# Kernel tuning notes

Measured on AMD Instinct MI355X. Metric: run time of the kernel, lower is better.

Reference implementation:

```python
import jax, jax.numpy as jnp
import numpy as np

# ---- module constants (from init_kwargs) ----
EMBED_DIM = 384
NUM_HYPEREDGES = 128
TOPK = 64
SPATIAL_SHAPE = (16, 32, 32)  # D, H, W -> N = 16384
SPACING = (2.0, 1.0, 1.0)
SPATIAL_WEIGHT = 0.1
B, N, C = 4, 16 * 32 * 32, EMBED_DIM


def _l2norm(x, axis=-1, eps=1e-12):
    n = jnp.linalg.norm(x, axis=axis, keepdims=True)
    return x / jnp.maximum(n, eps)


def _get_3d_coords():
    D, H, W = SPATIAL_SHAPE
    z = jnp.arange(D, dtype=jnp.float32) * SPACING[0]
    y = jnp.arange(H, dtype=jnp.float32) * SPACING[1]
    x = jnp.arange(W, dtype=jnp.float32) * SPACING[2]
    zz, yy, xx = jnp.meshgrid(z, y, x, indexing='ij')
    return jnp.stack([zz, yy, xx], axis=-1).reshape(-1, 3)  # (N, 3)


def setup_inputs() -> dict:
    key = jax.random.key(0)
    k1, k2 = jax.random.split(key)
    node_features = jax.random.normal(k1, (B, N, C), dtype=jnp.float32)
    class_token = jax.random.normal(k2, (1, 1, C), dtype=jnp.float32)
    temperature = jnp.ones((1,), dtype=jnp.float32) * 0.07
    return {"node_features": node_features, "class_token": class_token, "temperature": temperature}


def reference(node_features, class_token, temperature):
    Ne = NUM_HYPEREDGES
    w = SPATIAL_WEIGHT
    temp = temperature[0]

    nodes_n = _l2norm(node_features)                      # (B, N, C)

    # Step 1: center sampling by semantic similarity to class token
    ct_n = _l2norm(jnp.broadcast_to(class_token, (B, 1, C)))
    scores = jnp.einsum('boc,bnc->bn', ct_n, nodes_n) / temp  # (B, N)
    _, center_idx = jax.lax.top_k(scores, Ne)             # (B, Ne)

    # Gather centers and compute cosine sim of every center vs all nodes
    centers = jnp.take_along_axis(node_features, center_idx[:, :, None], axis=1)  # (B, Ne, C)
    centers_n = _l2norm(centers)
    sem_sim = jnp.einsum('bec,bnc->ben', centers_n, nodes_n) / temp  # (B, Ne, N)

    # Spatial bias (normalized distance from each center voxel)
    coords = _get_3d_coords()                             # (N, 3)
    center_coords = coords[center_idx]                    # (B, Ne, 3)
    diff = coords[None, None, :, :] - center_coords[:, :, None, :]  # (B, Ne, N, 3)
    dist = jnp.linalg.norm(diff, axis=-1)                 # (B, Ne, N)
    dist = dist / (jnp.max(dist, axis=-1, keepdims=True) + 1e-8)
    combined = (1.0 - w) * sem_sim + w * (1.0 - dist)     # (B, Ne, N)

    # Per-hyperedge top-K neighbors -> incidence matrix H (B, N, Ne)
    _, nbr_idx = jax.lax.top_k(combined, TOPK)            # (B, Ne, K)
    b_ix = jnp.arange(B)[:, None, None]
    e_ix = jnp.arange(Ne)[None, :, None]
    Hmat = jnp.zeros((B, N, Ne), dtype=node_features.dtype)
    Hmat = Hmat.at[b_ix, nbr_idx, e_ix].set(1.0)
    return Hmat
```

## Files before the change

kernel.cpp:

```cpp
#include <hip/hip_runtime.h>
#include <math.h>

#define BB 4
#define NN 16384
#define CC 384
#define NE 128
#define KK 64
#define CAP 1024

typedef unsigned short ushort_t;
typedef __attribute__((ext_vector_type(8))) short bf16x8;
typedef __attribute__((ext_vector_type(4))) float f32x4;
#define MFMA(a, b, c) __builtin_amdgcn_mfma_f32_16x16x32_bf16(a, b, c, 0, 0, 0)

__device__ inline unsigned fkey(float f) {
    unsigned b = __float_as_uint(f);
    return (b & 0x80000000u) ? ~b : (b | 0x80000000u);
}
__device__ inline ushort_t bf16rne(float f) {
    unsigned u = __float_as_uint(f);
    unsigned r = u + 0x7FFFu + ((u >> 16) & 1u);
    return (ushort_t)(r >> 16);
}
__device__ inline float bf16tof(ushort_t h) {
    return __uint_as_float(((unsigned)h) << 16);
}
__device__ inline void cvt2(float fa, float fb, unsigned& hp, unsigned& lp) {
    unsigned ua = __float_as_uint(fa), ub = __float_as_uint(fb);
    unsigned ra = ua + 0x8000u, rb = ub + 0x8000u;
    hp = (ra >> 16) | (rb & 0xFFFF0000u);
    float ha = __uint_as_float(ra & 0xFFFF0000u);
    float hb = __uint_as_float(rb & 0xFFFF0000u);
    float la = fa - ha, lb = fb - hb;
    unsigned lra = __float_as_uint(la) + 0x8000u;
    unsigned lrb = __float_as_uint(lb) + 0x8000u;
    lp = (lra >> 16) | (lrb & 0xFFFF0000u);
}

__device__ inline void load_lds16(const ushort_t* g, ushort_t* l) {
    __builtin_amdgcn_global_load_lds(
        (const __attribute__((address_space(1))) unsigned int*)(const void*)g,
        (__attribute__((address_space(3))) unsigned int*)(void*)l, 16, 0, 0);
}

__device__ inline void bin_select4k(const unsigned* hist, int t, int* wsum,
                                    int* sh_bin, int* sh_r, int r) {
    int base = t * 4;
    int c0 = hist[base], c1 = hist[base + 1], c2 = hist[base + 2], c3 = hist[base + 3];
    int csum = c0 + c1 + c2 + c3;
    int lane = t & 63, wid = t >> 6;
    int x = csum;
#pragma unroll
    for (int off = 1; off < 64; off <<= 1) {
        int v = __shfl_down(x, off, 64);
        if (lane + off < 64) x += v;
    }
    if (lane == 0) wsum[wid] = x;
    __syncthreads();
    int after = 0;
    for (int w2 = wid + 1; w2 < 16; ++w2) after += wsum[w2];
    int S = x - csum + after;
    if (S < r && S + c3 >= r) { *sh_bin = base + 3; *sh_r = r - S; }
    S += c3;
    if (S < r && S + c2 >= r) { *sh_bin = base + 2; *sh_r = r - S; }
    S += c2;
    if (S < r && S + c1 >= r) { *sh_bin = base + 1; *sh_r = r - S; }
    S += c1;
    if (S < r && S + c0 >= r) { *sh_bin = base + 0; *sh_r = r - S; }
    __syncthreads();
}

__global__ __launch_bounds__(256) void k_scores(const float* __restrict__ nf,
                                                const float* __restrict__ ct,
                                                unsigned* __restrict__ keys,
                                                float* __restrict__ invn) {
    int wave = threadIdx.x >> 6;
    int lane = threadIdx.x & 63;
    int row  = blockIdx.x * 4 + wave;
    const float* x = nf + (size_t)row * CC;
    float4 a  = ((const float4*)x)[lane];
    float2 c2 = ((const float2*)(x + 256))[lane];
    float4 ta = ((const float4*)ct)[lane];
    float2 tc = ((const float2*)(ct + 256))[lane];
    float ss = a.x*a.x + a.y*a.y + a.z*a.z + a.w*a.w + c2.x*c2.x + c2.y*c2.y;
    float dt = ta.x*a.x + ta.y*a.y + ta.z*a.z + ta.w*a.w + tc.x*c2.x + tc.y*c2.y;
#pragma unroll
    for (int off = 32; off; off >>= 1) {
        ss += __shfl_xor(ss, off, 64);
        dt += __shfl_xor(dt, off, 64);
    }
    if (lane == 0) {
        float inv = 1.0f / fmaxf(sqrtf(ss), 1e-12f);
        invn[row] = inv;
        keys[row] = fkey(dt * inv);
    }
}

__global__ __launch_bounds__(1024) void k_top128(const unsigned* __restrict__ keys,
                                                 const float* __restrict__ nf,
                                                 const float* __restrict__ invn,
                                                 float* __restrict__ meta,
                                                 ushort_t* __restrict__ Ahi,
                                                 ushort_t* __restrict__ Alo) {
    __shared__ unsigned hist[4096];
    __shared__ int wsum[16];
    __shared__ int sh_bin, sh_r;
    __shared__ unsigned cu[NE];
    __shared__ int cil[NE];
    __shared__ unsigned eqk[CAP];
    __shared__ int eqi[CAP];
    __shared__ int cnt_gt, cnt_eq;
    __shared__ int ocid[NE];
    int b = blockIdx.x;
    int t = threadIdx.x;
    const uint4* rowv = (const uint4*)(keys + b * NN);
    if (t == 0) { cnt_gt = 0; cnt_eq = 0; }
    ((uint4*)hist)[t] = make_uint4(0, 0, 0, 0);
    __syncthreads();
    uint4 u0 = rowv[t], u1 = rowv[t + 1024], u2 = rowv[t + 2048], u3 = rowv[t + 3072];
    atomicAdd(&hist[u0.x >> 20], 1u); atomicAdd(&hist[u0.y >> 20], 1u);
    atomicAdd(&hist[u0.z >> 20], 1u); atomicAdd(&hist[u0.w >> 20], 1u);
    atomicAdd(&hist[u1.x >> 20], 1u); atomicAdd(&hist[u1.y >> 20], 1u);
    atomicAdd(&hist[u1.z >> 20], 1u); atomicAdd(&hist[u1.w >> 20], 1u);
    atomicAdd(&hist[u2.x >> 20], 1u); atomicAdd(&hist[u2.y >> 20], 1u);
    atomicAdd(&hist[u2.z >> 20], 1u); atomicAdd(&hist[u2.w >> 20], 1u);
    atomicAdd(&hist[u3.x >> 20], 1u); atomicAdd(&hist[u3.y >> 20], 1u);
    atomicAdd(&hist[u3.z >> 20], 1u); atomicAdd(&hist[u3.w >> 20], 1u);
    __syncthreads();
    bin_select4k(hist, t, wsum, &sh_bin, &sh_r, NE);
    unsigned bin = (unsigned)sh_bin;
    int r = sh_r;
#define EMIT128(uu, nn) { unsigned tb = (uu) >> 20; \
    if (tb > bin) { int p = atomicAdd(&cnt_gt, 1); cu[p] = (uu); cil[p] = (nn); } \
    else if (tb == bin) { int p = atomicAdd(&cnt_eq, 1); if (p < CAP) { eqk[p] = (uu); eqi[p] = (nn); } } }
    EMIT128(u0.x, 4*t+0); EMIT128(u0.y, 4*t+1); EMIT128(u0.z, 4*t+2); EMIT128(u0.w, 4*t+3);
    EMIT128(u1.x, 4096+4*t+0); EMIT128(u1.y, 4096+4*t+1); EMIT128(u1.z, 4096+4*t+2); EMIT128(u1.w, 4096+4*t+3);
    EMIT128(u2.x, 8192+4*t+0); EMIT128(u2.y, 8192+4*t+1); EMIT128(u2.z, 8192+4*t+2); EMIT128(u2.w, 8192+4*t+3);
    EMIT128(u3.x, 12288+4*t+0); EMIT128(u3.y, 12288+4*t+1); EMIT128(u3.z, 12288+4*t+2); EMIT128(u3.w, 12288+4*t+3);
#undef EMIT128
    __syncthreads();
    int ne = cnt_eq < CAP ? cnt_eq : CAP;
    for (int i = t; i < ne; i += 1024) {
        unsigned ki = eqk[i]; int ii = eqi[i], rk = 0;
        for (int j = 0; j < ne; ++j) {
            unsigned kj = eqk[j];
            rk += (kj > ki) || (kj == ki && eqi[j] < ii);
        }
        if (rk < r) { cu[cnt_gt + rk] = ki; cil[cnt_gt + rk] = ii; }
    }
    __syncthreads();
    if (t < NE) {
        unsigned mu = cu[t]; int mi = cil[t], rk = 0;
#pragma unroll 4
        for (int j = 0; j < NE; ++j) {
            unsigned ou = cu[j]; int oi = cil[j];
            rk += (ou > mu) || (ou == mu && oi < mi);
        }
        ocid[rk] = mi;
    }
    __syncthreads();
    if (t < NE) {
        int ci = ocid[t];
        float zc = (float)(ci >> 10) * 2.0f;
        float yc = (float)((ci >> 5) & 31);
        float xc = (float)(ci & 31);
        float mz = fmaxf(zc * zc, (30.f - zc) * (30.f - zc));
        float my = fmaxf(yc * yc, (31.f - yc) * (31.f - yc));
        float mx = fmaxf(xc * xc, (31.f - xc) * (31.f - xc));
        float md = sqrtf(mz + my + mx);
        int be = b * NE + t;
        meta[be * 4 + 0] = zc;
        meta[be * 4 + 1] = yc;
        meta[be * 4 + 2] = xc;
        meta[be * 4 + 3] = 1.0f / (md + 1e-8f);
    }
    {
        int wid2 = t >> 6, lane2 = t & 63;
        ushort_t* dh = Ahi + (size_t)b * NE * CC;
        ushort_t* dl = Alo + (size_t)b * NE * CC;
        for (int e = wid2; e < NE; e += 16) {
            int ci = ocid[e];
            float inv = invn[b * NN + ci];
            const float* src = nf + ((size_t)b * NN + ci) * CC;
            float4 a  = ((const float4*)src)[lane2];
            float2 cv = ((const float2*)(src + 256))[lane2];
            a.x *= inv; a.y *= inv; a.z *= inv; a.w *= inv;
            cv.x *= inv; cv.y *= inv;
            ushort4 h4; ushort2 h2;
            h4.x = bf16rne(a.x); h4.y = bf16rne(a.y); h4.z = bf16rne(a.z); h4.w = bf16rne(a.w);
            h2.x = bf16rne(cv.x); h2.y = bf16rne(cv.y);
            ushort4 l4; ushort2 l2;
            l4.x = bf16rne(a.x - bf16tof(h4.x)); l4.y = bf16rne(a.y - bf16tof(h4.y));
            l4.z = bf16rne(a.z - bf16tof(h4.z)); l4.w = bf16rne(a.w - bf16tof(h4.w));
            l2.x = bf16rne(cv.x - bf16tof(h2.x)); l2.y = bf16rne(cv.y - bf16tof(h2.y));
            int off4 = ((lane2 >> 1) * NE + e) * 8 + 4 * (lane2 & 1);
            int off2 = ((32 + (lane2 >> 2)) * NE + e) * 8 + 2 * (lane2 & 3);
            *(ushort4*)(dh + off4) = h4;
            *(ushort2*)(dh + off2) = h2;
            *(ushort4*)(dl + off4) = l4;
            *(ushort2*)(dl + off2) = l2;
        }
    }
}

__global__ __launch_bounds__(256, 2) void k_gemm(const float* __restrict__ nf,
                                                 const ushort_t* __restrict__ Ahi,
                                                 const ushort_t* __restrict__ Alo,
                                                 const float* __restrict__ invn,
                                                 const float* __restrict__ meta,
                                                 const float* __restrict__ temp,
                                                 unsigned* __restrict__ outk) {
    __shared__ ushort_t Ah[2][4096], Al[2][4096];
    __shared__ ushort_t Bh[2][4160], Bl[2][4160];
    __shared__ float ms[NE * 4];
    __shared__ float invs_s[128];
    int b  = blockIdx.y;
    int n0 = blockIdx.x * 128;
    int t  = threadIdx.x;
    int w = t >> 6, lane = t & 63, quad = lane >> 4, mrow = lane & 15;
    int wr = w >> 1, wc = w & 1;
    for (int i = t; i < NE * 4; i += 256) ms[i] = meta[b * NE * 4 + i];
    if (t < 128) invs_s[t] = invn[b * NN + n0 + t];
    f32x4 acc[4][4];
#pragma unroll
    for (int i = 0; i < 4; ++i)
#pragma unroll
        for (int j = 0; j < 4; ++j) acc[i][j] = (f32x4)0.f;
    const ushort_t* Abh = Ahi + (size_t)b * NE * CC;
    const ushort_t* Abl = Alo + (size_t)b * NE * CC;
    const ushort_t* ah0 = Abh + w * 1024 + lane * 8;
    const ushort_t* ah1 = ah0 + 512;
    const ushort_t* al0 = Abl + w * 1024 + lane * 8;
    const ushort_t* al1 = al0 + 512;
    int bn = t >> 2, bk8 = t & 3;
    int sb0 = bk8 * 130 + bn, sb1 = sb0 + 64;
    const float* bs0 = nf + ((size_t)b * NN + n0 + bn) * CC + bk8 * 8;
    const float* bs1 = bs0 + (size_t)64 * CC;
    float4 s0a, s0b, s0c, s0d;
    float4 s1a, s1b, s1c, s1d;
    load_lds16(ah0, &Ah[0][w * 1024]);
    load_lds16(ah1, &Ah[0][w * 1024 + 512]);
    load_lds16(al0, &Al[0][w * 1024]);
    load_lds16(al1, &Al[0][w * 1024 + 512]);
    __builtin_amdgcn_sched_barrier(0);
    s0a = ((const float4*)bs0)[0]; s0b = ((const float4*)bs0)[1];
    s0c = ((const float4*)bs1)[0]; s0d = ((const float4*)bs1)[1];
    s1a = ((const float4*)(bs0 + 32))[0]; s1b = ((const float4*)(bs0 + 32))[1];
    s1c = ((const float4*)(bs1 + 32))[0]; s1d = ((const float4*)(bs1 + 32))[1];
    {
        uint4 ph, pl;
        cvt2(s0a.x, s0a.y, ph.x, pl.x); cvt2(s0a.z, s0a.w, ph.y, pl.y);
        cvt2(s0b.x, s0b.y, ph.z, pl.z); cvt2(s0b.z, s0b.w, ph.w, pl.w);
        *(uint4*)&Bh[0][sb0 * 8] = ph; *(uint4*)&Bl[0][sb0 * 8] = pl;
        cvt2(s0c.x, s0c.y, ph.x, pl.x); cvt2(s0c.z, s0c.w, ph.y, pl.y);
        cvt2(s0d.x, s0d.y, ph.z, pl.z); cvt2(s0d.z, s0d.w, ph.w, pl.w);
        *(uint4*)&Bh[0][sb1 * 8] = ph; *(uint4*)&Bl[0][sb1 * 8] = pl;
    }
    s0a = ((const float4*)(bs0 + 64))[0]; s0b = ((const float4*)(bs0 + 64))[1];
    s0c = ((const float4*)(bs1 + 64))[0]; s0d = ((const float4*)(bs1 + 64))[1];
    asm volatile("s_waitcnt vmcnt(8) lgkmcnt(0)" ::: "memory");
    __builtin_amdgcn_s_barrier();
    __builtin_amdgcn_sched_barrier(0);

#define GSTEP(KS, CUR, NXT, SA, SB, SC, SD)                                     \
    {                                                                           \
        if ((KS) < 11) {                                                        \
            const int kt = ((KS) + 1) * 32;                                     \
            load_lds16(ah0 + kt * 128, &Ah[NXT][w * 1024]);                     \
            load_lds16(ah1 + kt * 128, &Ah[NXT][w * 1024 + 512]);               \
            load_lds16(al0 + kt * 128, &Al[NXT][w * 1024]);                     \
            load_lds16(al1 + kt * 128, &Al[NXT][w * 1024 + 512]);               \
            __builtin_amdgcn_sched_barrier(0);                                  \
            uint4 ph, pl;                                                       \
            cvt2(SA.x, SA.y, ph.x, pl.x); cvt2(SA.z, SA.w, ph.y, pl.y);         \
            cvt2(SB.x, SB.y, ph.z, pl.z); cvt2(SB.z, SB.w, ph.w, pl.w);         \
            *(uint4*)&Bh[NXT][sb0 * 8] = ph; *(uint4*)&Bl[NXT][sb0 * 8] = pl;   \
            cvt2(SC.x, SC.y, ph.x, pl.x); cvt2(SC.z, SC.w, ph.y, pl.y);         \
            cvt2(SD.x, SD.y, ph.z, pl.z); cvt2(SD.z, SD.w, ph.w, pl.w);         \
            *(uint4*)&Bh[NXT][sb1 * 8] = ph; *(uint4*)&Bl[NXT][sb1 * 8] = pl;   \
            const int kt3 = ((KS) + 3 <= 11 ? (KS) + 3 : 11) * 32;              \
            SA = ((const float4*)(bs0 + kt3))[0];                               \
            SB = ((const float4*)(bs0 + kt3))[1];                               \
            SC = ((const float4*)(bs1 + kt3))[0];                               \
            SD = ((const float4*)(bs1 + kt3))[1];                               \
        }                                                                       \
        bf16x8 afh[4], afl[4], bfh[4], bfl[4];                                  \
        _Pragma("unroll") for (int i = 0; i < 4; ++i) {                         \
            int m = wr * 64 + i * 16 + mrow;                                    \
            afh[i] = *(const bf16x8*)&Ah[CUR][(quad * 128 + m) * 8];            \
            afl[i] = *(const bf16x8*)&Al[CUR][(quad * 128 + m) * 8];            \
        }                                                                       \
        _Pragma("unroll") for (int j = 0; j < 4; ++j) {                         \
            int n = wc * 64 + j * 16 + mrow;                                    \
            bfh[j] = *(const bf16x8*)&Bh[CUR][(quad * 130 + n) * 8];            \
            bfl[j] = *(const bf16x8*)&Bl[CUR][(quad * 130 + n) * 8];            \
        }                                                                       \
        __builtin_amdgcn_s_setprio(1);                                          \
        _Pragma("unroll") for (int i = 0; i < 4; ++i)                           \
        _Pragma("unroll") for (int j = 0; j < 4; ++j) {                         \
            acc[i][j] = MFMA(afh[i], bfh[j], acc[i][j]);                        \
            acc[i][j] = MFMA(afh[i], bfl[j], acc[i][j]);                        \
            acc[i][j] = MFMA(afl[i], bfh[j], acc[i][j]);                        \
        }                                                                       \
        __builtin_amdgcn_s_setprio(0);                                          \
        if ((KS) < 11) {                                                        \
            asm volatile("s_waitcnt vmcnt(4) lgkmcnt(0)" ::: "memory");         \
            __builtin_amdgcn_s_barrier();                                       \
            __builtin_amdgcn_sched_barrier(0);                                  \
        }                                                                       \
    }

    GSTEP(0, 0, 1, s1a, s1b, s1c, s1d)
    GSTEP(1, 1, 0, s0a, s0b, s0c, s0d)
    GSTEP(2, 0, 1, s1a, s1b, s1c, s1d)
    GSTEP(3, 1, 0, s0a, s0b, s0c, s0d)
    GSTEP(4, 0, 1, s1a, s1b, s1c, s1d)
    GSTEP(5, 1, 0, s0a, s0b, s0c, s0d)
    GSTEP(6, 0, 1, s1a, s1b, s1c, s1d)
    GSTEP(7, 1, 0, s0a, s0b, s0c, s0d)
    GSTEP(8, 0, 1, s1a, s1b, s1c, s1d)
    GSTEP(9, 1, 0, s0a, s0b, s0c, s0d)
    GSTEP(10, 0, 1, s1a, s1b, s1c, s1d)
    GSTEP(11, 1, 0, s0a, s0b, s0c, s0d)
#undef GSTEP

    float scale = 0.9f / temp[0];
#pragma unroll
    for (int j = 0; j < 4; ++j) {
        int nloc = wc * 64 + j * 16 + mrow;
        int n = n0 + nloc;
        float invnn = invs_s[nloc];
        float zf = (float)(n >> 10) * 2.0f;
        float yf = (float)((n >> 5) & 31);
        float xf = (float)(n & 31);
#pragma unroll
        for (int i = 0; i < 4; ++i) {
#pragma unroll
            for (int r = 0; r < 4; ++r) {
                int el = wr * 64 + i * 16 + quad * 4 + r;
                float zc = ms[el * 4 + 0], yc = ms[el * 4 + 1], xc = ms[el * 4 + 2], ivd = ms[el * 4 + 3];
                float dz = zf - zc, dy = yf - yc, dx = xf - xc;
                float dist = sqrtf(dz * dz + dy * dy + dx * dx);
                float v = scale * invnn * acc[i][j][r] + 0.1f * (1.0f - dist * ivd);
                outk[((size_t)(b * NE + el)) * NN + n] = fkey(v);
            }
        }
    }
}

__global__ __launch_bounds__(512) void k_top64(const unsigned* __restrict__ comb,
                                               unsigned* __restrict__ bmg) {
    __shared__ unsigned hist[4096];
    __shared__ unsigned bm[512];
    __shared__ int wsum[8];
    __shared__ int sh_bin, sh_r;
    __shared__ unsigned eqk[CAP];
    __shared__ int eqi[CAP];
    __shared__ int cnt_eq;
    int be = blockIdx.x;
    int t  = threadIdx.x;
    const uint4* rowv = (const uint4*)(comb + (size_t)be * NN);
    if (t == 0) cnt_eq = 0;
    ((uint4*)hist)[t] = make_uint4(0, 0, 0, 0);
    ((uint4*)hist)[t + 512] = make_uint4(0, 0, 0, 0);
    if (t < 128) ((uint4*)bm)[t] = make_uint4(0, 0, 0, 0);
    __syncthreads();
    uint4 u[8];
#pragma unroll
    for (int i = 0; i < 8; ++i) u[i] = rowv[t + 512 * i];
#pragma unroll
    for (int i = 0; i < 8; ++i) {
        atomicAdd(&hist[u[i].x >> 20], 1u); atomicAdd(&hist[u[i].y >> 20], 1u);
        atomicAdd(&hist[u[i].z >> 20], 1u); atomicAdd(&hist[u[i].w >> 20], 1u);
    }
    __syncthreads();
    {
        int base = t * 8;
        int c[8]; int csum = 0;
#pragma unroll
        for (int i = 0; i < 8; ++i) { c[i] = hist[base + i]; csum += c[i]; }
        int lane = t & 63, wid = t >> 6;
        int x = csum;
#pragma unroll
        for (int off = 1; off < 64; off <<= 1) {
            int v = __shfl_down(x, off, 64);
            if (lane + off < 64) x += v;
        }
        if (lane == 0) wsum[wid] = x;
        __syncthreads();
        int after = 0;
        for (int w2 = wid + 1; w2 < 8; ++w2) after += wsum[w2];
        int S = x - csum + after;
#pragma unroll
        for (int i = 7; i >= 0; --i) {
            if (S < KK && S + c[i] >= KK) { sh_bin = base + i; sh_r = KK - S; }
            S += c[i];
        }
        __syncthreads();
    }
    unsigned bin = (unsigned)sh_bin;
    int r = sh_r;
#define EMIT64(uu, nn) { unsigned tb = (uu) >> 20; \
    if (tb > bin) { atomicOr(&bm[(nn) >> 5], 1u << ((nn) & 31)); } \
    else if (tb == bin) { int p = atomicAdd(&cnt_eq, 1); if (p < CAP) { eqk[p] = (uu); eqi[p] = (nn); } } }
#pragma unroll
    for (int i = 0; i < 8; ++i) {
        int nb = 4 * (t + 512 * i);
        EMIT64(u[i].x, nb + 0); EMIT64(u[i].y, nb + 1);
        EMIT64(u[i].z, nb + 2); EMIT64(u[i].w, nb + 3);
    }
#undef EMIT64
    __syncthreads();
    int ne = cnt_eq < CAP ? cnt_eq : CAP;
    for (int i = t; i < ne; i += 512) {
        unsigned ki = eqk[i]; int ii = eqi[i], rk = 0;
        for (int j = 0; j < ne; ++j) {
            unsigned kj = eqk[j];
            rk += (kj > ki) || (kj == ki && eqi[j] < ii);
        }
        if (rk < r) atomicOr(&bm[ii >> 5], 1u << (ii & 31));
    }
    __syncthreads();
    if (t < 128) ((uint4*)(bmg + (size_t)be * 512))[t] = ((uint4*)bm)[t];
}

__global__ __launch_bounds__(256) void k_expand(const unsigned* __restrict__ bmg,
                                                float* __restrict__ H) {
    __shared__ unsigned wl[256];
    int b  = blockIdx.y;
    int n0 = blockIdx.x * 64;
    int t  = threadIdx.x;
    int w0 = n0 >> 5;
    wl[t] = bmg[((size_t)b * NE + (t >> 1)) * 512 + w0 + (t & 1)];
    __syncthreads();
    float4* dst = (float4*)(H + ((size_t)b * NN + n0) * NE);
#pragma unroll
    for (int i = 0; i < 8; ++i) {
        int flat = t + 256 * i;
        int nl = flat >> 5, f4 = flat & 31;
        int wsel = nl >> 5, bit = nl & 31;
        int e = f4 * 4;
        float4 v;
        v.x = (float)((wl[(e + 0) * 2 + wsel] >> bit) & 1u);
        v.y = (float)((wl[(e + 1) * 2 + wsel] >> bit) & 1u);
        v.z = (float)((wl[(e + 2) * 2 + wsel] >> bit) & 1u);
        v.w = (float)((wl[(e + 3) * 2 + wsel] >> bit) & 1u);
        dst[flat] = v;
    }
}

extern "C" void kernel_launch(void* const* d_in, const int* in_sizes, int n_in,
                              void* d_out, int out_size, void* d_ws, size_t ws_size,
                              hipStream_t stream) {
    const float* nf   = (const float*)d_in[0];
    const float* ct   = (const float*)d_in[1];
    const float* temp = (const float*)d_in[2];
    float* out = (float*)d_out;

    unsigned* keys = (unsigned*)d_ws;
    float* invn    = (float*)(keys + BB * NN);
    float* meta    = invn + BB * NN;
    ushort_t* Ahi  = (ushort_t*)(meta + BB * NE * 4);
    ushort_t* Alo  = Ahi + (size_t)BB * NE * CC;
    unsigned* bmg  = (unsigned*)(Alo + (size_t)BB * NE * CC);

    k_scores <<<BB * NN / 4, 256, 0, stream>>>(nf, ct, keys, invn);
    k_top128 <<<BB, 1024, 0, stream>>>(keys, nf, invn, meta, Ahi, Alo);
    k_gemm   <<<dim3(NN / 128, BB), 256, 0, stream>>>(nf, Ahi, Alo, invn, meta, temp, (unsigned*)out);
    k_top64  <<<BB * NE, 512, 0, stream>>>((const unsigned*)out, bmg);
    k_expand <<<dim3(NN / 64, BB), 256, 0, stream>>>(bmg, out);
}
```

Measured before the change: 242.6 us.

## Grid-stride score kernel, deeper GEMM prefetch wait, 1024-thread top64 blocks

k_scores becomes a grid-stride loop over row groups with a fixed 2048-block grid, so the class-token loads happen once per thread instead of once per block. The GEMM pipeline waitcnt is relaxed from vmcnt(4) to vmcnt(8), letting more global loads stay in flight across the barrier. k_top64 moves to 1024 threads per row, reusing the shared bin_select4k helper and holding fewer values per thread. These changes trade block-launch overhead and register pressure against occupancy, and the vmcnt change depends on the actual load count per step being correct.

```diff
diff --git a/kernel.cpp b/kernel.cpp
--- a/kernel.cpp
+++ b/kernel.cpp
@@ -76,23 +76,25 @@
                                                 float* __restrict__ invn) {
     int wave = threadIdx.x >> 6;
     int lane = threadIdx.x & 63;
-    int row  = blockIdx.x * 4 + wave;
-    const float* x = nf + (size_t)row * CC;
-    float4 a  = ((const float4*)x)[lane];
-    float2 c2 = ((const float2*)(x + 256))[lane];
     float4 ta = ((const float4*)ct)[lane];
     float2 tc = ((const float2*)(ct + 256))[lane];
-    float ss = a.x*a.x + a.y*a.y + a.z*a.z + a.w*a.w + c2.x*c2.x + c2.y*c2.y;
-    float dt = ta.x*a.x + ta.y*a.y + ta.z*a.z + ta.w*a.w + tc.x*c2.x + tc.y*c2.y;
-#pragma unroll
-    for (int off = 32; off; off >>= 1) {
-        ss += __shfl_xor(ss, off, 64);
-        dt += __shfl_xor(dt, off, 64);
-    }
-    if (lane == 0) {
-        float inv = 1.0f / fmaxf(sqrtf(ss), 1e-12f);
-        invn[row] = inv;
-        keys[row] = fkey(dt * inv);
+    for (int rg = blockIdx.x; rg < BB * NN / 4; rg += gridDim.x) {
+        int row = rg * 4 + wave;
+        const float* x = nf + (size_t)row * CC;
+        float4 a  = ((const float4*)x)[lane];
+        float2 c2 = ((const float2*)(x + 256))[lane];
+        float ss = a.x*a.x + a.y*a.y + a.z*a.z + a.w*a.w + c2.x*c2.x + c2.y*c2.y;
+        float dt = ta.x*a.x + ta.y*a.y + ta.z*a.z + ta.w*a.w + tc.x*c2.x + tc.y*c2.y;
+#pragma unroll
+        for (int off = 32; off; off >>= 1) {
+            ss += __shfl_xor(ss, off, 64);
+            dt += __shfl_xor(dt, off, 64);
+        }
+        if (lane == 0) {
+            float inv = 1.0f / fmaxf(sqrtf(ss), 1e-12f);
+            invn[row] = inv;
+            keys[row] = fkey(dt * inv);
+        }
     }
 }
 
@@ -304,7 +306,7 @@
         }                                                                       \
         __builtin_amdgcn_s_setprio(0);                                          \
         if ((KS) < 11) {                                                        \
-            asm volatile("s_waitcnt vmcnt(4) lgkmcnt(0)" ::: "memory");         \
+            asm volatile("s_waitcnt vmcnt(8) lgkmcnt(0)" ::: "memory");         \
             __builtin_amdgcn_s_barrier();                                       \
             __builtin_amdgcn_sched_barrier(0);                                  \
         }                                                                       \
@@ -348,11 +350,11 @@
     }
 }
 
-__global__ __launch_bounds__(512) void k_top64(const unsigned* __restrict__ comb,
-                                               unsigned* __restrict__ bmg) {
+__global__ __launch_bounds__(1024) void k_top64(const unsigned* __restrict__ comb,
+                                                unsigned* __restrict__ bmg) {
     __shared__ unsigned hist[4096];
     __shared__ unsigned bm[512];
-    __shared__ int wsum[8];
+    __shared__ int wsum[16];
     __shared__ int sh_bin, sh_r;
     __shared__ unsigned eqk[CAP];
     __shared__ int eqi[CAP];
@@ -362,57 +364,32 @@
     const uint4* rowv = (const uint4*)(comb + (size_t)be * NN);
     if (t == 0) cnt_eq = 0;
     ((uint4*)hist)[t] = make_uint4(0, 0, 0, 0);
-    ((uint4*)hist)[t + 512] = make_uint4(0, 0, 0, 0);
     if (t < 128) ((uint4*)bm)[t] = make_uint4(0, 0, 0, 0);
     __syncthreads();
-    uint4 u[8];
-#pragma unroll
-    for (int i = 0; i < 8; ++i) u[i] = rowv[t + 512 * i];
-#pragma unroll
-    for (int i = 0; i < 8; ++i) {
-        atomicAdd(&hist[u[i].x >> 20], 1u); atomicAdd(&hist[u[i].y >> 20], 1u);
-        atomicAdd(&hist[u[i].z >> 20], 1u); atomicAdd(&hist[u[i].w >> 20], 1u);
-    }
-    __syncthreads();
-    {
-        int base = t * 8;
-        int c[8]; int csum = 0;
-#pragma unroll
-        for (int i = 0; i < 8; ++i) { c[i] = hist[base + i]; csum += c[i]; }
-        int lane = t & 63, wid = t >> 6;
-        int x = csum;
-#pragma unroll
-        for (int off = 1; off < 64; off <<= 1) {
-            int v = __shfl_down(x, off, 64);
-            if (lane + off < 64) x += v;
-        }
-        if (lane == 0) wsum[wid] = x;
-        __syncthreads();
-        int after = 0;
-        for (int w2 = wid + 1; w2 < 8; ++w2) after += wsum[w2];
-        int S = x - csum + after;
-#pragma unroll
-        for (int i = 7; i >= 0; --i) {
-            if (S < KK && S + c[i] >= KK) { sh_bin = base + i; sh_r = KK - S; }
-            S += c[i];
-        }
-        __syncthreads();
-    }
+    uint4 u0 = rowv[t], u1 = rowv[t + 1024], u2 = rowv[t + 2048], u3 = rowv[t + 3072];
+    atomicAdd(&hist[u0.x >> 20], 1u); atomicAdd(&hist[u0.y >> 20], 1u);
+    atomicAdd(&hist[u0.z >> 20], 1u); atomicAdd(&hist[u0.w >> 20], 1u);
+    atomicAdd(&hist[u1.x >> 20], 1u); atomicAdd(&hist[u1.y >> 20], 1u);
+    atomicAdd(&hist[u1.z >> 20], 1u); atomicAdd(&hist[u1.w >> 20], 1u);
+    atomicAdd(&hist[u2.x >> 20], 1u); atomicAdd(&hist[u2.y >> 20], 1u);
+    atomicAdd(&hist[u2.z >> 20], 1u); atomicAdd(&hist[u2.w >> 20], 1u);
+    atomicAdd(&hist[u3.x >> 20], 1u); atomicAdd(&hist[u3.y >> 20], 1u);
+    atomicAdd(&hist[u3.z >> 20], 1u); atomicAdd(&hist[u3.w >> 20], 1u);
+    __syncthreads();
+    bin_select4k(hist, t, wsum, &sh_bin, &sh_r, KK);
     unsigned bin = (unsigned)sh_bin;
     int r = sh_r;
 #define EMIT64(uu, nn) { unsigned tb = (uu) >> 20; \
     if (tb > bin) { atomicOr(&bm[(nn) >> 5], 1u << ((nn) & 31)); } \
     else if (tb == bin) { int p = atomicAdd(&cnt_eq, 1); if (p < CAP) { eqk[p] = (uu); eqi[p] = (nn); } } }
-#pragma unroll
-    for (int i = 0; i < 8; ++i) {
-        int nb = 4 * (t + 512 * i);
-        EMIT64(u[i].x, nb + 0); EMIT64(u[i].y, nb + 1);
-        EMIT64(u[i].z, nb + 2); EMIT64(u[i].w, nb + 3);
-    }
+    EMIT64(u0.x, 4*t+0); EMIT64(u0.y, 4*t+1); EMIT64(u0.z, 4*t+2); EMIT64(u0.w, 4*t+3);
+    EMIT64(u1.x, 4096+4*t+0); EMIT64(u1.y, 4096+4*t+1); EMIT64(u1.z, 4096+4*t+2); EMIT64(u1.w, 4096+4*t+3);
+    EMIT64(u2.x, 8192+4*t+0); EMIT64(u2.y, 8192+4*t+1); EMIT64(u2.z, 8192+4*t+2); EMIT64(u2.w, 8192+4*t+3);
+    EMIT64(u3.x, 12288+4*t+0); EMIT64(u3.y, 12288+4*t+1); EMIT64(u3.z, 12288+4*t+2); EMIT64(u3.w, 12288+4*t+3);
 #undef EMIT64
     __syncthreads();
     int ne = cnt_eq < CAP ? cnt_eq : CAP;
-    for (int i = t; i < ne; i += 512) {
+    for (int i = t; i < ne; i += 1024) {
         unsigned ki = eqk[i]; int ii = eqi[i], rk = 0;
         for (int j = 0; j < ne; ++j) {
             unsigned kj = eqk[j];
@@ -464,9 +441,9 @@
     ushort_t* Alo  = Ahi + (size_t)BB * NE * CC;
     unsigned* bmg  = (unsigned*)(Alo + (size_t)BB * NE * CC);
 
-    k_scores <<<BB * NN / 4, 256, 0, stream>>>(nf, ct, keys, invn);
+    k_scores <<<2048, 256, 0, stream>>>(nf, ct, keys, invn);
     k_top128 <<<BB, 1024, 0, stream>>>(keys, nf, invn, meta, Ahi, Alo);
     k_gemm   <<<dim3(NN / 128, BB), 256, 0, stream>>>(nf, Ahi, Alo, invn, meta, temp, (unsigned*)out);
-    k_top64  <<<BB * NE, 512, 0, stream>>>((const unsigned*)out, bmg);
+    k_top64  <<<BB * NE, 1024, 0, stream>>>((const unsigned*)out, bmg);
     k_expand <<<dim3(NN / 64, BB), 256, 0, stream>>>(bmg, out);
 }
```

After: 245.3 us. About the same (+1.1%).
